# Kernel tuning notes

Hardware: AMD Instinct MI355X
Metric: run time of the kernel (lower is better)

Reference implementation:

```python
import jax, jax.numpy as jnp
import numpy as np

N, DIN, D, K0, NC = 32768, 768, 512, 128, 2
KS = [128, 64, 32, 16]  # prototype counts per stage (num_protos // 2**i)
NEG_SLOPE = 0.01


def _lin(x, W, b):
    # torch nn.Linear: W is [out, in]
    return x @ W.T + b


def _ln(x, g, b):
    m = x.mean(-1, keepdims=True)
    v = ((x - m) ** 2).mean(-1, keepdims=True)
    return (x - m) * jax.lax.rsqrt(v + 1e-5) * g + b


def setup_inputs() -> dict:
    key = jax.random.key(0)
    ks = jax.random.split(key, 40)
    s = 0.02

    def nrm(k, shp, sc=s):
        return jax.random.normal(k, shp, jnp.float32) * sc

    inp = {}
    inp["data"] = jax.random.normal(ks[0], (N, DIN), jnp.float32)
    inp["prototypes"] = jax.random.normal(ks[1], (K0, DIN), jnp.float32)
    inp["W_pp"] = nrm(ks[2], (D, DIN)); inp["b_pp"] = jnp.zeros((D,), jnp.float32)
    inp["W_cp"] = nrm(ks[3], (D, DIN)); inp["b_cp"] = jnp.zeros((D,), jnp.float32)
    inp["sim_scale"] = jnp.ones((1,), jnp.float32)
    # 3 enhancer MLPs + layernorms (stacked, same shapes)
    inp["enh_w1"] = nrm(ks[4], (3, D, D)); inp["enh_b1"] = jnp.zeros((3, D), jnp.float32)
    inp["enh_w2"] = nrm(ks[5], (3, D, D)); inp["enh_b2"] = jnp.zeros((3, D), jnp.float32)
    inp["ln_g"] = jnp.ones((3, D), jnp.float32); inp["ln_b"] = jnp.zeros((3, D), jnp.float32)
    # ProtoReducers: Mlp along K axis; fc1 [inK,inK], fc2 [outK,inK]
    ki = 6
    for i in range(3):
        inK, outK = KS[i], KS[i + 1]
        inp[f"red_w1_{i}"] = nrm(ks[ki], (inK, inK)); ki += 1
        inp[f"red_b1_{i}"] = jnp.zeros((inK,), jnp.float32)
        inp[f"red_w2_{i}"] = nrm(ks[ki], (outK, inK)); ki += 1
        inp[f"red_b2_{i}"] = jnp.zeros((outK,), jnp.float32)
    inp["W_proc"] = nrm(ks[20], (D, D)); inp["b_proc"] = jnp.zeros((D,), jnp.float32)
    inp["g_an"] = jnp.ones((D,), jnp.float32); inp["b_an"] = jnp.zeros((D,), jnp.float32)
    inp["W_t"] = nrm(ks[21], (D, D)); inp["b_t"] = jnp.zeros((D,), jnp.float32)
    inp["W_g"] = nrm(ks[22], (D, D)); inp["b_g"] = jnp.zeros((D,), jnp.float32)
    inp["W_s"] = nrm(ks[23], (1, D)); inp["b_s"] = jnp.zeros((1,), jnp.float32)
    inp["W_h"] = nrm(ks[24], (D, D)); inp["b_h"] = jnp.zeros((D,), jnp.float32)
    inp["W_c"] = nrm(ks[25], (NC, D)); inp["b_c"] = jnp.zeros((NC,), jnp.float32)
    return inp


def reference(data, prototypes, W_pp, b_pp, W_cp, b_cp, sim_scale,
              enh_w1, enh_b1, enh_w2, enh_b2, ln_g, ln_b,
              red_w1_0, red_b1_0, red_w2_0, red_b2_0,
              red_w1_1, red_b1_1, red_w2_1, red_b2_1,
              red_w1_2, red_b1_2, red_w2_2, red_b2_2,
              W_proc, b_proc, g_an, b_an,
              W_t, b_t, W_g, b_g, W_s, b_s, W_h, b_h, W_c, b_c):
    # patch / prototype projections (Linear + LeakyReLU)
    P = jax.nn.leaky_relu(_lin(data, W_pp, b_pp), NEG_SLOPE)        # [N, D]
    C = jax.nn.leaky_relu(_lin(prototypes, W_cp, b_cp), NEG_SLOPE)  # [K0, D]
    # denom = max(1e-6, tau * similarity_scale.item()); tau=1, no grad through scale
    denom = jnp.maximum(1e-6, jax.lax.stop_gradient(sim_scale)[0])
    reds = [(red_w1_0, red_b1_0, red_w2_0, red_b2_0),
            (red_w1_1, red_b1_1, red_w2_1, red_b2_1),
            (red_w1_2, red_b1_2, red_w2_2, red_b2_2)]
    for i in range(3):
        # L2 similarity: -cdist(P, C) computed as a GEMM
        d2 = (jnp.sum(P * P, -1, keepdims=True) + jnp.sum(C * C, -1)[None, :]
              - 2.0 * (P @ C.T))
        sim = -jnp.sqrt(jnp.maximum(d2, 1e-12))                     # [N, K]
        A = jax.nn.softmax(sim / denom, axis=1)                     # soft routing
        ctx = A @ C                                                 # [N, D]
        P = _ln(P + ctx, ln_g[i], ln_b[i])
        P = P + _lin(jax.nn.relu(_lin(P, enh_w1[i], enh_b1[i])), enh_w2[i], enh_b2[i])
        # ProtoReducer: Mlp over K axis (operate on C.T of shape [D, K])
        w1, b1, w2, b2 = reds[i]
        Ct = _lin(jax.nn.relu(_lin(C.T, w1, b1)), w2, b2)           # [D, Kout]
        C = Ct.T
    Z = jnp.concatenate([P, C], axis=0)                             # [N+16, D]
    Z = jax.nn.relu(_lin(Z, W_proc, b_proc))
    Z = _ln(Z, g_an, b_an)
    # gated attention MIL pooling
    t = jnp.tanh(_lin(Z, W_t, b_t))
    g = jax.nn.sigmoid(_lin(Z, W_g, b_g))
    scores = _lin(t * g, W_s, b_s)                                  # [N+16, 1]
    Aw = jax.nn.softmax(scores, axis=0)
    bag = Aw.T @ Z                                                  # [1, D]
    h = jax.nn.relu(_lin(bag, W_h, b_h))
    logits = _lin(h, W_c, b_c)                                      # [1, 2]
    return logits
```

## Files before the change

kernel.cpp:

```cpp
#include <hip/hip_runtime.h>
#include <math.h>

typedef _Float16 f16x8 __attribute__((ext_vector_type(8)));
typedef _Float16 f16x4 __attribute__((ext_vector_type(4)));
typedef float f32x4 __attribute__((ext_vector_type(4)));

#define TBM 256
#define TBN 128
#define TBK 32

#define AS1 __attribute__((address_space(1)))
#define AS3 __attribute__((address_space(3)))

__device__ __forceinline__ void gll16(const _Float16* g, _Float16* l)
{
    __builtin_amdgcn_global_load_lds((const AS1 unsigned int*)g,
                                     (AS3 unsigned int*)l, 16, 0, 0);
}

__device__ __forceinline__ int xcd_swz(int d, int nwg)
{
    int q = nwg >> 3, r = nwg & 7;
    int x = d & 7, idx = d >> 3;
    int base = x < r ? x * (q + 1) : r * (q + 1) + (x - r) * q;
    return base + idx;
}

__device__ __forceinline__ float fsigmoid(float x)
{
    return __builtin_amdgcn_rcpf(1.f + __expf(-x));
}
__device__ __forceinline__ float ftanh(float x)
{
    float ax = fabsf(x);
    float e = __expf(-2.f * ax);
    float t = (1.f - e) * __builtin_amdgcn_rcpf(1.f + e);
    return copysignf(t, x);
}

template<int ACT, bool F16OUT>
__global__ __launch_bounds__(256)
void dot_k(const float* __restrict__ X, const float* __restrict__ W,
           const float* __restrict__ bias, void* __restrict__ Yv,
           int M, int K)
{
    int gw = (blockIdx.x * 256 + threadIdx.x) >> 6;
    int lane = threadIdx.x & 63;
    if (gw >= M * 512) return;
    int r = gw >> 9, n = gw & 511;
    const float* xr = X + (size_t)r * K;
    const float* wr = W + (size_t)n * K;
    float d = 0.f;
    for (int t = 0; t < K; t += 256) {
        float4 a = *(const float4*)(xr + t + lane * 4);
        float4 b = *(const float4*)(wr + t + lane * 4);
        d += a.x * b.x + a.y * b.y + a.z * b.z + a.w * b.w;
    }
#pragma unroll
    for (int o = 32; o; o >>= 1) d += __shfl_xor(d, o);
    if (lane == 0) {
        float v = d + bias[n];
        if (ACT == 1) v = v > 0.f ? v : 0.01f * v;
        else if (ACT == 2) v = fmaxf(v, 0.f);
        if (F16OUT) ((_Float16*)Yv)[(size_t)r * 512 + n] = (_Float16)v;
        else        ((float*)Yv)[(size_t)r * 512 + n] = v;
    }
}

__global__ __launch_bounds__(256)
void cvtC2_k(const float* __restrict__ C, _Float16* __restrict__ Ch,
             _Float16* __restrict__ CTh, float* __restrict__ Csq, int Kin)
{
    int w = threadIdx.x >> 6, lane = threadIdx.x & 63;
    int row = blockIdx.x * 4 + w;
    if (row >= Kin) return;
    float4 a = *(const float4*)(C + (size_t)row * 512 + lane * 8);
    float4 b = *(const float4*)(C + (size_t)row * 512 + lane * 8 + 4);
    f16x8 h;
    h[0] = (_Float16)a.x; h[1] = (_Float16)a.y; h[2] = (_Float16)a.z; h[3] = (_Float16)a.w;
    h[4] = (_Float16)b.x; h[5] = (_Float16)b.y; h[6] = (_Float16)b.z; h[7] = (_Float16)b.w;
    *(f16x8*)(Ch + (size_t)row * 512 + lane * 8) = h;
    float s = 0.f;
#pragma unroll
    for (int q = 0; q < 8; q++) {
        float f = (float)h[q];
        s += f * f;
        CTh[(size_t)(lane * 8 + q) * Kin + row] = h[q];
    }
#pragma unroll
    for (int o = 32; o; o >>= 1) s += __shfl_xor(s, o);
    if (lane == 0) Csq[row] = s;
}

template<int MODE, int ACT, bool SQ>
__global__ __launch_bounds__(512)
void mgemm(const _Float16* __restrict__ A, const _Float16* __restrict__ B,
           const float* __restrict__ bias, _Float16* __restrict__ Yh,
           float* __restrict__ Psq, int M, int K, int Nout)
{
    __shared__ _Float16 As[2][TBM * TBK];
    __shared__ _Float16 Bs[2][TBN * TBK];
    const int tid = threadIdx.x;
    const int lane = tid & 63;
    const int wid = tid >> 6;
    const int wr = wid >> 1, wc = wid & 1;

    int bid = xcd_swz(blockIdx.y * gridDim.x + blockIdx.x, gridDim.x * gridDim.y);
    const int m0 = (bid / gridDim.x) * TBM;
    const int n0 = (bid % gridDim.x) * TBN;

    f32x4 acc[4][4] = {};
    const int nt = K / TBK;

    const int lrow = lane >> 2;
    const int lk = (lane & 3) * 8;

    auto stage = [&](int t, int buf) {
        const int k0 = t * TBK;
#pragma unroll
        for (int q = 0; q < 2; q++) {
            int c = wid * 2 + q;
            int r = c * 16 + lrow;
            int am = min(m0 + r, M - 1);
            gll16(A + (size_t)am * K + k0 + lk, &As[buf][c * 512]);
        }
        {
            int c = wid;
            int r = c * 16 + lrow;
            int bn = min(n0 + r, Nout - 1);
            gll16(B + (size_t)bn * K + k0 + lk, &Bs[buf][c * 512]);
        }
    };

    stage(0, 0);
    __syncthreads();
    for (int t = 0; t < nt; ++t) {
        const int cur = t & 1;
        if (t + 1 < nt) stage(t + 1, cur ^ 1);
        f16x8 af[4], bf[4];
#pragma unroll
        for (int mi = 0; mi < 4; mi++)
            af[mi] = *(const f16x8*)(&As[cur][(wr * 64 + mi * 16 + (lane & 15)) * TBK + (lane >> 4) * 8]);
#pragma unroll
        for (int nj = 0; nj < 4; nj++)
            bf[nj] = *(const f16x8*)(&Bs[cur][(wc * 64 + nj * 16 + (lane & 15)) * TBK + (lane >> 4) * 8]);
#pragma unroll
        for (int mi = 0; mi < 4; mi++)
#pragma unroll
            for (int nj = 0; nj < 4; nj++)
                acc[mi][nj] = __builtin_amdgcn_mfma_f32_16x16x32_f16(af[mi], bf[nj], acc[mi][nj], 0, 0, 0);
        __syncthreads();
    }

    _Float16* eb = &As[0][0];
    const int g = lane >> 4;
#pragma unroll
    for (int p = 0; p < 2; p++) {
        if (p) __syncthreads();
        if ((wr >> 1) == p) {
#pragma unroll
            for (int nj = 0; nj < 4; nj++) {
                int col = wc * 64 + nj * 16 + (lane & 15);
                float bv = bias ? bias[n0 + col] : 0.f;
#pragma unroll
                for (int mi = 0; mi < 4; mi++)
#pragma unroll
                    for (int r = 0; r < 4; r++) {
                        int lr = (wr & 1) * 64 + mi * 16 + g * 4 + r;
                        float v = acc[mi][nj][r] + bv;
                        if (MODE == 0) {
                            if (ACT == 1) v = v > 0.f ? v : 0.01f * v;
                            else if (ACT == 2) v = fmaxf(v, 0.f);
                        }
                        eb[lr * 128 + col] = (_Float16)v;
                    }
            }
        }
        __syncthreads();
        int t4 = tid * 4;
        int lr = t4 >> 4;
        int cbase = (t4 & 15) * 8;
        int m = m0 + p * 128 + lr;
        float sq = 0.f;
        if (m < M) {
#pragma unroll
            for (int q = 0; q < 4; q++) {
                int c0 = cbase + q * 8;
                f16x8 hv = *(f16x8*)(eb + lr * 128 + c0);
                size_t gidx = (size_t)m * Nout + n0 + c0;
                if (MODE == 1) {
                    f16x8 old = *(f16x8*)(Yh + gidx);
                    f16x8 nw;
#pragma unroll
                    for (int e = 0; e < 8; e++) {
                        float s = (float)old[e] + (float)hv[e];
                        nw[e] = (_Float16)s;
                    }
                    *(f16x8*)(Yh + gidx) = nw;
                    hv = nw;
                } else {
                    *(f16x8*)(Yh + gidx) = hv;
                }
                if (SQ) {
#pragma unroll
                    for (int e = 0; e < 8; e++) { float f = (float)hv[e]; sq += f * f; }
                }
            }
        }
        if (SQ) {
            sq += __shfl_xor(sq, 1);
            sq += __shfl_xor(sq, 2);
            if ((lane & 3) == 0 && m < M) atomicAdd(&Psq[m], sq);
        }
    }
}

__global__ __launch_bounds__(512)
void ctxln_k(const _Float16* __restrict__ A, const _Float16* __restrict__ CT,
             const float* __restrict__ g, const float* __restrict__ b,
             _Float16* __restrict__ Ph, int M, int Kin)
{
    __shared__ _Float16 As[2][128 * TBK];
    __shared__ _Float16 Bs[2][512 * TBK];
    const int tid = threadIdx.x;
    const int lane = tid & 63;
    const int wid = tid >> 6;
    const int wr = wid >> 2, wc = wid & 3;
    const int m0 = blockIdx.y * 128;

    f32x4 acc[4][8] = {};
    const int nt = Kin / TBK;

    const int lrow = lane >> 2;
    const int lk = (lane & 3) * 8;

    auto stage = [&](int t, int buf) {
        const int k0 = t * TBK;
        {
            int r = wid * 16 + lrow;
            gll16(A + (size_t)(m0 + r) * Kin + k0 + lk, &As[buf][wid * 512]);
        }
#pragma unroll
        for (int q = 0; q < 4; q++) {
            int c = wid * 4 + q;
            int n = c * 16 + lrow;
            gll16(CT + (size_t)n * Kin + k0 + lk, &Bs[buf][c * 512]);
        }
    };

    stage(0, 0);
    __syncthreads();
    for (int t = 0; t < nt; ++t) {
        const int cur = t & 1;
        if (t + 1 < nt) stage(t + 1, cur ^ 1);
        f16x8 af[4], bf[8];
#pragma unroll
        for (int mi = 0; mi < 4; mi++)
            af[mi] = *(const f16x8*)(&As[cur][(wr * 64 + mi * 16 + (lane & 15)) * TBK + (lane >> 4) * 8]);
#pragma unroll
        for (int nj = 0; nj < 8; nj++)
            bf[nj] = *(const f16x8*)(&Bs[cur][(wc * 128 + nj * 16 + (lane & 15)) * TBK + (lane >> 4) * 8]);
#pragma unroll
        for (int mi = 0; mi < 4; mi++)
#pragma unroll
            for (int nj = 0; nj < 8; nj++)
                acc[mi][nj] = __builtin_amdgcn_mfma_f32_16x16x32_f16(af[mi], bf[nj], acc[mi][nj], 0, 0, 0);
        __syncthreads();
    }

    _Float16* eb = &Bs[0][0];
    const int gq = lane >> 4;
#pragma unroll
    for (int p = 0; p < 2; p++) {
        if (p) __syncthreads();
        if (wr == p) {
#pragma unroll
            for (int nj = 0; nj < 8; nj++) {
                int col = wc * 128 + nj * 16 + (lane & 15);
#pragma unroll
                for (int mi = 0; mi < 4; mi++)
#pragma unroll
                    for (int r = 0; r < 4; r++) {
                        int lr = mi * 16 + gq * 4 + r;
                        eb[lr * 512 + col] = (_Float16)acc[mi][nj][r];
                    }
            }
        }
        __syncthreads();
#pragma unroll
        for (int rr = 0; rr < 8; rr++) {
            int lr = wid * 8 + rr;
            int m = m0 + p * 64 + lr;
            f16x8 cv = *(f16x8*)(eb + lr * 512 + lane * 8);
            f16x8 pv = *(const f16x8*)(Ph + (size_t)m * 512 + lane * 8);
            float v[8];
            float s = 0.f, ss = 0.f;
#pragma unroll
            for (int q = 0; q < 8; q++) {
                v[q] = (float)pv[q] + (float)cv[q];
                s += v[q]; ss += v[q] * v[q];
            }
#pragma unroll
            for (int o = 32; o; o >>= 1) { s += __shfl_xor(s, o); ss += __shfl_xor(ss, o); }
            float mean = s * (1.f / 512.f);
            float var = ss * (1.f / 512.f) - mean * mean;
            float inv = 1.f / sqrtf(var + 1e-5f);
            int d0 = lane * 8;
            f16x8 o8;
#pragma unroll
            for (int q = 0; q < 8; q++)
                o8[q] = (_Float16)((v[q] - mean) * inv * g[d0 + q] + b[d0 + q]);
            *(f16x8*)(Ph + (size_t)m * 512 + d0) = o8;
        }
    }
}

__global__ __launch_bounds__(512)
void procln_k(const _Float16* __restrict__ A, const _Float16* __restrict__ W,
              const float* __restrict__ bias, const float* __restrict__ g,
              const float* __restrict__ b, _Float16* __restrict__ Zh, int M)
{
    __shared__ _Float16 As[2][128 * TBK];
    __shared__ _Float16 Bs[2][512 * TBK];
    const int tid = threadIdx.x;
    const int lane = tid & 63;
    const int wid = tid >> 6;
    const int wr = wid >> 2, wc = wid & 3;
    const int m0 = blockIdx.y * 128;
    const int K = 512;

    f32x4 acc[4][8] = {};
    const int nt = K / TBK;

    const int lrow = lane >> 2;
    const int lk = (lane & 3) * 8;

    auto stage = [&](int t, int buf) {
        const int k0 = t * TBK;
        {
            int r = wid * 16 + lrow;
            gll16(A + (size_t)(m0 + r) * K + k0 + lk, &As[buf][wid * 512]);
        }
#pragma unroll
        for (int q = 0; q < 4; q++) {
            int c = wid * 4 + q;
            int n = c * 16 + lrow;
            gll16(W + (size_t)n * K + k0 + lk, &Bs[buf][c * 512]);
        }
    };

    stage(0, 0);
    __syncthreads();
    for (int t = 0; t < nt; ++t) {
        const int cur = t & 1;
        if (t + 1 < nt) stage(t + 1, cur ^ 1);
        f16x8 af[4], bf[8];
#pragma unroll
        for (int mi = 0; mi < 4; mi++)
            af[mi] = *(const f16x8*)(&As[cur][(wr * 64 + mi * 16 + (lane & 15)) * TBK + (lane >> 4) * 8]);
#pragma unroll
        for (int nj = 0; nj < 8; nj++)
            bf[nj] = *(const f16x8*)(&Bs[cur][(wc * 128 + nj * 16 + (lane & 15)) * TBK + (lane >> 4) * 8]);
#pragma unroll
        for (int mi = 0; mi < 4; mi++)
#pragma unroll
            for (int nj = 0; nj < 8; nj++)
                acc[mi][nj] = __builtin_amdgcn_mfma_f32_16x16x32_f16(af[mi], bf[nj], acc[mi][nj], 0, 0, 0);
        __syncthreads();
    }

    _Float16* eb = &Bs[0][0];
    const int gq = lane >> 4;
#pragma unroll
    for (int p = 0; p < 2; p++) {
        if (p) __syncthreads();
        if (wr == p) {
#pragma unroll
            for (int nj = 0; nj < 8; nj++) {
                int col = wc * 128 + nj * 16 + (lane & 15);
                float bv = bias[col];
#pragma unroll
                for (int mi = 0; mi < 4; mi++)
#pragma unroll
                    for (int r = 0; r < 4; r++) {
                        int lr = mi * 16 + gq * 4 + r;
                        eb[lr * 512 + col] = (_Float16)fmaxf(acc[mi][nj][r] + bv, 0.f);
                    }
            }
        }
        __syncthreads();
#pragma unroll
        for (int rr = 0; rr < 8; rr++) {
            int lr = wid * 8 + rr;
            int m = m0 + p * 64 + lr;
            f16x8 cv = *(f16x8*)(eb + lr * 512 + lane * 8);
            float v[8];
            float s = 0.f, ss = 0.f;
#pragma unroll
            for (int q = 0; q < 8; q++) {
                v[q] = (float)cv[q];
                s += v[q]; ss += v[q] * v[q];
            }
#pragma unroll
            for (int o = 32; o; o >>= 1) { s += __shfl_xor(s, o); ss += __shfl_xor(ss, o); }
            float mean = s * (1.f / 512.f);
            float var = ss * (1.f / 512.f) - mean * mean;
            float inv = 1.f / sqrtf(var + 1e-5f);
            int d0 = lane * 8;
            f16x8 o8;
#pragma unroll
            for (int q = 0; q < 8; q++)
                o8[q] = (_Float16)((v[q] - mean) * inv * g[d0 + q] + b[d0 + q]);
            *(f16x8*)(Zh + (size_t)m * 512 + d0) = o8;
        }
    }
}

__global__ __launch_bounds__(512)
void gatgemm(const _Float16* __restrict__ A, const _Float16* __restrict__ B1,
             const _Float16* __restrict__ B2, const float* __restrict__ c1,
             const float* __restrict__ c2, const float* __restrict__ Ws,
             float* __restrict__ scr, int M, int K, int Nout)
{
    __shared__ _Float16 As[2][TBM * TBK];
    __shared__ _Float16 B1s[2][TBN * TBK];
    __shared__ _Float16 B2s[2][TBN * TBK];
    const int tid = threadIdx.x;
    const int lane = tid & 63;
    const int wid = tid >> 6;
    const int wr = wid >> 1, wc = wid & 1;

    int bid = xcd_swz(blockIdx.y * gridDim.x + blockIdx.x, gridDim.x * gridDim.y);
    const int m0 = (bid / gridDim.x) * TBM;
    const int n0 = (bid % gridDim.x) * TBN;

    f32x4 acc1[4][4] = {};
    f32x4 acc2[4][4] = {};
    const int nt = K / TBK;

    const int lrow = lane >> 2;
    const int lk = (lane & 3) * 8;

    auto stage = [&](int t, int buf) {
        const int k0 = t * TBK;
#pragma unroll
        for (int q = 0; q < 2; q++) {
            int c = wid * 2 + q;
            int r = c * 16 + lrow;
            int am = min(m0 + r, M - 1);
            gll16(A + (size_t)am * K + k0 + lk, &As[buf][c * 512]);
        }
        {
            int c = wid;
            int r = c * 16 + lrow;
            int bn = min(n0 + r, Nout - 1);
            gll16(B1 + (size_t)bn * K + k0 + lk, &B1s[buf][c * 512]);
            gll16(B2 + (size_t)bn * K + k0 + lk, &B2s[buf][c * 512]);
        }
    };

    stage(0, 0);
    __syncthreads();
    for (int t = 0; t < nt; ++t) {
        const int cur = t & 1;
        if (t + 1 < nt) stage(t + 1, cur ^ 1);
        f16x8 af[4], bf1[4], bf2[4];
#pragma unroll
        for (int mi = 0; mi < 4; mi++)
            af[mi] = *(const f16x8*)(&As[cur][(wr * 64 + mi * 16 + (lane & 15)) * TBK + (lane >> 4) * 8]);
#pragma unroll
        for (int nj = 0; nj < 4; nj++) {
            int ro = (wc * 64 + nj * 16 + (lane & 15)) * TBK + (lane >> 4) * 8;
            bf1[nj] = *(const f16x8*)(&B1s[cur][ro]);
            bf2[nj] = *(const f16x8*)(&B2s[cur][ro]);
        }
#pragma unroll
        for (int mi = 0; mi < 4; mi++)
#pragma unroll
            for (int nj = 0; nj < 4; nj++) {
                acc1[mi][nj] = __builtin_amdgcn_mfma_f32_16x16x32_f16(af[mi], bf1[nj], acc1[mi][nj], 0, 0, 0);
                acc2[mi][nj] = __builtin_amdgcn_mfma_f32_16x16x32_f16(af[mi], bf2[nj], acc2[mi][nj], 0, 0, 0);
            }
        __syncthreads();
    }

    const int g = lane >> 4;
    float wsv[4];
#pragma unroll
    for (int nj = 0; nj < 4; nj++)
        wsv[nj] = Ws[n0 + wc * 64 + nj * 16 + (lane & 15)];
#pragma unroll
    for (int mi = 0; mi < 4; mi++) {
#pragma unroll
        for (int r = 0; r < 4; r++) {
            float p = 0.f;
#pragma unroll
            for (int nj = 0; nj < 4; nj++) {
                int col = n0 + wc * 64 + nj * 16 + (lane & 15);
                float t1 = ftanh(acc1[mi][nj][r] + c1[col]);
                float g1 = fsigmoid(acc2[mi][nj][r] + c2[col]);
                p += t1 * g1 * wsv[nj];
            }
#pragma unroll
            for (int o = 1; o < 16; o <<= 1) p += __shfl_xor(p, o);
            if ((lane & 15) == 0) {
                int m = m0 + wr * 64 + mi * 16 + g * 4 + r;
                if (m < M) atomicAdd(&scr[m], p);
            }
        }
    }
}

#define SBM 128
__global__ __launch_bounds__(256)
void simgemm(const _Float16* __restrict__ A, const _Float16* __restrict__ B,
             const float* __restrict__ Psq, const float* __restrict__ Csq,
             const float* __restrict__ sscale, _Float16* __restrict__ Ah,
             int M, int K, int Kin)
{
    __shared__ _Float16 As[2][SBM * TBK];
    __shared__ _Float16 Bs[2][SBM * TBK];
    __shared__ float redmx[2][SBM];
    __shared__ float redsm[2][SBM];
    const int tid = threadIdx.x;
    const int lane = tid & 63;
    const int wid = tid >> 6;
    const int wr = wid >> 1, wc = wid & 1;
    const int m0 = blockIdx.y * SBM;

    f32x4 acc[4][4] = {};
    const int nt = K / TBK;
    const int lrow = lane >> 2;
    const int lk = (lane & 3) * 8;

    auto stage = [&](int t, int buf) {
        const int k0 = t * TBK;
#pragma unroll
        for (int q = 0; q < 2; q++) {
            int c = wid * 2 + q;
            int r = c * 16 + lrow;
            int am = min(m0 + r, M - 1);
            gll16(A + (size_t)am * K + k0 + lk, &As[buf][c * 512]);
            if (c * 16 < Kin) {
                int bn = min(r, Kin - 1);
                gll16(B + (size_t)bn * K + k0 + lk, &Bs[buf][c * 512]);
            }
        }
    };

    stage(0, 0);
    __syncthreads();
    for (int t = 0; t < nt; ++t) {
        const int cur = t & 1;
        if (t + 1 < nt) stage(t + 1, cur ^ 1);
        f16x8 af[4], bf[4];
#pragma unroll
        for (int mi = 0; mi < 4; mi++)
            af[mi] = *(const f16x8*)(&As[cur][(wr * 64 + mi * 16 + (lane & 15)) * TBK + (lane >> 4) * 8]);
#pragma unroll
        for (int nj = 0; nj < 4; nj++)
            bf[nj] = *(const f16x8*)(&Bs[cur][(wc * 64 + nj * 16 + (lane & 15)) * TBK + (lane >> 4) * 8]);
#pragma unroll
        for (int mi = 0; mi < 4; mi++)
#pragma unroll
            for (int nj = 0; nj < 4; nj++)
                acc[mi][nj] = __builtin_amdgcn_mfma_f32_16x16x32_f16(af[mi], bf[nj], acc[mi][nj], 0, 0, 0);
        __syncthreads();
    }

    const float denom = fmaxf(1e-6f, sscale[0]);
    const int colbase = wc * 64 + (lane & 15);
    const int g = lane >> 4;
    float cc[4];
#pragma unroll
    for (int nj = 0; nj < 4; nj++) {
        int n = colbase + nj * 16;
        cc[nj] = (n < Kin) ? Csq[n] : 0.f;
    }

#pragma unroll
    for (int mi = 0; mi < 4; mi++) {
#pragma unroll
        for (int r = 0; r < 4; r++) {
            int row = wr * 64 + mi * 16 + g * 4 + r;
            float pp = Psq[m0 + row];
            float mx = -INFINITY;
#pragma unroll
            for (int nj = 0; nj < 4; nj++) {
                int n = colbase + nj * 16;
                float v = -INFINITY;
                if (n < Kin)
                    v = -sqrtf(fmaxf(pp + cc[nj] - 2.f * acc[mi][nj][r], 1e-12f)) / denom;
                acc[mi][nj][r] = v;
                mx = fmaxf(mx, v);
            }
#pragma unroll
            for (int o = 1; o < 16; o <<= 1) mx = fmaxf(mx, __shfl_xor(mx, o));
            if ((lane & 15) == 0) redmx[wc][row] = mx;
        }
    }
    __syncthreads();

#pragma unroll
    for (int mi = 0; mi < 4; mi++) {
#pragma unroll
        for (int r = 0; r < 4; r++) {
            int row = wr * 64 + mi * 16 + g * 4 + r;
            float mx = fmaxf(redmx[0][row], redmx[1][row]);
            float s = 0.f;
#pragma unroll
            for (int nj = 0; nj < 4; nj++) {
                int n = colbase + nj * 16;
                float e = (n < Kin) ? __expf(acc[mi][nj][r] - mx) : 0.f;
                acc[mi][nj][r] = e;
                s += e;
            }
#pragma unroll
            for (int o = 1; o < 16; o <<= 1) s += __shfl_xor(s, o);
            if ((lane & 15) == 0) redsm[wc][row] = s;
        }
    }
    __syncthreads();

#pragma unroll
    for (int mi = 0; mi < 4; mi++) {
#pragma unroll
        for (int r = 0; r < 4; r++) {
            int row = wr * 64 + mi * 16 + g * 4 + r;
            float inv = __builtin_amdgcn_rcpf(redsm[0][row] + redsm[1][row]);
            int m = m0 + row;
#pragma unroll
            for (int nj = 0; nj < 4; nj++) {
                int n = colbase + nj * 16;
                if (n < Kin)
                    Ah[(size_t)m * Kin + n] = (_Float16)(acc[mi][nj][r] * inv);
            }
        }
    }
}

__global__ __launch_bounds__(256)
void cvt_k(const float* __restrict__ x, _Float16* __restrict__ y, int n)
{
    int i = (blockIdx.x * 256 + threadIdx.x) * 4;
    if (i < n) {
        float4 v = *(const float4*)(x + i);
        f16x4 h = { (_Float16)v.x, (_Float16)v.y, (_Float16)v.z, (_Float16)v.w };
        *(f16x4*)(y + i) = h;
    }
}

__global__ __launch_bounds__(256)
void ln_k(const _Float16* __restrict__ X, const _Float16* __restrict__ R,
          const float* __restrict__ g, const float* __restrict__ b,
          _Float16* __restrict__ Yh, int M)
{
    int wid = threadIdx.x >> 6, lane = threadIdx.x & 63;
    int row = blockIdx.x * 4 + wid;
    if (row >= M) return;
    f16x8 a = *(const f16x8*)(X + (size_t)row * 512 + lane * 8);
    float v[8];
#pragma unroll
    for (int q = 0; q < 8; q++) v[q] = (float)a[q];
    if (R) {
        f16x8 c = *(const f16x8*)(R + (size_t)row * 512 + lane * 8);
#pragma unroll
        for (int q = 0; q < 8; q++) v[q] += (float)c[q];
    }
    float s = 0.f, ss = 0.f;
#pragma unroll
    for (int q = 0; q < 8; q++) { s += v[q]; ss += v[q] * v[q]; }
#pragma unroll
    for (int o = 32; o; o >>= 1) { s += __shfl_xor(s, o); ss += __shfl_xor(ss, o); }
    float mean = s * (1.f / 512.f);
    float var = ss * (1.f / 512.f) - mean * mean;
    float inv = 1.f / sqrtf(var + 1e-5f);
    int d0 = lane * 8;
    f16x8 o8;
#pragma unroll
    for (int q = 0; q < 8; q++)
        o8[q] = (_Float16)((v[q] - mean) * inv * g[d0 + q] + b[d0 + q]);
    *(f16x8*)(Yh + (size_t)row * 512 + d0) = o8;
}

__global__ __launch_bounds__(256)
void red1_k(const float* __restrict__ C, const float* __restrict__ w1,
            const float* __restrict__ b1, float* __restrict__ H1, int Kin)
{
    int d = blockIdx.x * 256 + threadIdx.x;
    int j = blockIdx.y;
    float acc = b1[j];
    for (int k = 0; k < Kin; k++) acc = fmaf(C[(size_t)k * 512 + d], w1[(size_t)j * Kin + k], acc);
    H1[(size_t)j * 512 + d] = fmaxf(acc, 0.f);
}

__global__ __launch_bounds__(256)
void red2_k(const float* __restrict__ H1, const float* __restrict__ w2,
            const float* __restrict__ b2, float* __restrict__ Cn,
            _Float16* __restrict__ Chn, _Float16* __restrict__ CThn,
            float* __restrict__ Csqn, int Kin, int Kout)
{
    int d = blockIdx.x * 256 + threadIdx.x;
    int j2 = blockIdx.y;
    float acc = b2[j2];
    for (int j = 0; j < Kin; j++) acc = fmaf(H1[(size_t)j * 512 + d], w2[(size_t)j2 * Kin + j], acc);
    Cn[(size_t)j2 * 512 + d] = acc;
    _Float16 h = (_Float16)acc;
    Chn[(size_t)j2 * 512 + d] = h;
    CThn[(size_t)d * Kout + j2] = h;
    float f = (float)h;
    float sq = f * f;
#pragma unroll
    for (int o = 32; o; o >>= 1) sq += __shfl_xor(sq, o);
    if ((threadIdx.x & 63) == 0) atomicAdd(&Csqn[j2], sq);
}

__global__ __launch_bounds__(1024)
void pool_k(float* __restrict__ s, float* __restrict__ scal, int M)
{
    __shared__ float sm[16];
    int tid = threadIdx.x, lane = tid & 63, wid = tid >> 6;
    float mx = -INFINITY;
    for (int i = tid * 4; i < M; i += 4096) {
        float4 a = *(const float4*)(s + i);
        mx = fmaxf(fmaxf(fmaxf(mx, a.x), fmaxf(a.y, a.z)), a.w);
    }
#pragma unroll
    for (int o = 32; o; o >>= 1) mx = fmaxf(mx, __shfl_xor(mx, o));
    if (lane == 0) sm[wid] = mx;
    __syncthreads();
    if (wid == 0) {
        float v = (lane < 16) ? sm[lane] : -INFINITY;
#pragma unroll
        for (int o = 8; o; o >>= 1) v = fmaxf(v, __shfl_xor(v, o));
        if (lane == 0) sm[0] = v;
    }
    __syncthreads();
    float gmax = sm[0];
    __syncthreads();
    float sum = 0.f;
    for (int i = tid * 4; i < M; i += 4096) {
        float4 a = *(const float4*)(s + i);
        float4 e;
        e.x = __expf(a.x - gmax); e.y = __expf(a.y - gmax);
        e.z = __expf(a.z - gmax); e.w = __expf(a.w - gmax);
        *(float4*)(s + i) = e;
        sum += e.x + e.y + e.z + e.w;
    }
#pragma unroll
    for (int o = 32; o; o >>= 1) sum += __shfl_xor(sum, o);
    if (lane == 0) sm[wid] = sum;
    __syncthreads();
    if (tid == 0) {
        float t = 0.f;
        for (int w = 0; w < 16; w++) t += sm[w];
        scal[0] = t;
    }
}

__global__ __launch_bounds__(256)
void bagp_k(const _Float16* __restrict__ Z, const float* __restrict__ w,
            float* __restrict__ PB, int M, int cs)
{
    int d = blockIdx.x * 256 + threadIdx.x;
    int chunk = blockIdx.y;
    int i0 = chunk * cs;
    int i1 = min(M, i0 + cs);
    float acc = 0.f;
    for (int i = i0; i < i1; i++) acc = fmaf(w[i], (float)Z[(size_t)i * 512 + d], acc);
    PB[(size_t)chunk * 512 + d] = acc;
}

__global__ __launch_bounds__(256)
void bagf_k(const float* __restrict__ PB, const float* __restrict__ scal,
            float* __restrict__ bag, int nchunk)
{
    int d = blockIdx.x * 256 + threadIdx.x;
    float acc = 0.f;
    for (int c = 0; c < nchunk; c++) acc += PB[(size_t)c * 512 + d];
    bag[d] = acc / scal[0];
}

__global__ __launch_bounds__(256)
void h_k(const float* __restrict__ bag, const float* __restrict__ Wh,
         const float* __restrict__ bh, float* __restrict__ h)
{
    int wid = threadIdx.x >> 6, lane = threadIdx.x & 63;
    int j = blockIdx.x * 4 + wid;
    const float* wr = Wh + (size_t)j * 512;
    float d = 0.f;
#pragma unroll
    for (int t = 0; t < 2; t++) {
        float4 a = *(const float4*)(wr + t * 256 + lane * 4);
        float4 bv = *(const float4*)(bag + t * 256 + lane * 4);
        d += a.x * bv.x + a.y * bv.y + a.z * bv.z + a.w * bv.w;
    }
#pragma unroll
    for (int o = 32; o; o >>= 1) d += __shfl_xor(d, o);
    if (lane == 0) h[j] = fmaxf(d + bh[j], 0.f);
}

__global__ __launch_bounds__(128)
void logit_k(const float* __restrict__ h, const float* __restrict__ Wc,
             const float* __restrict__ bc, float* __restrict__ out)
{
    int wid = threadIdx.x >> 6, lane = threadIdx.x & 63;
    const float* wr = Wc + (size_t)wid * 512;
    float d = 0.f;
#pragma unroll
    for (int t = 0; t < 2; t++) {
        float4 a = *(const float4*)(wr + t * 256 + lane * 4);
        float4 hv = *(const float4*)(h + t * 256 + lane * 4);
        d += a.x * hv.x + a.y * hv.y + a.z * hv.z + a.w * hv.w;
    }
#pragma unroll
    for (int o = 32; o; o >>= 1) d += __shfl_xor(d, o);
    if (lane == 0) out[wid] = d + bc[wid];
}

extern "C" void kernel_launch(void* const* d_in, const int* in_sizes, int n_in,
                              void* d_out, int out_size, void* d_ws, size_t ws_size,
                              hipStream_t stream)
{
    const float* data    = (const float*)d_in[0];
    const float* protos  = (const float*)d_in[1];
    const float* W_pp    = (const float*)d_in[2];
    const float* b_pp    = (const float*)d_in[3];
    const float* W_cp    = (const float*)d_in[4];
    const float* b_cp    = (const float*)d_in[5];
    const float* sscale  = (const float*)d_in[6];
    const float* enh_w1  = (const float*)d_in[7];
    const float* enh_b1  = (const float*)d_in[8];
    const float* enh_w2  = (const float*)d_in[9];
    const float* enh_b2  = (const float*)d_in[10];
    const float* ln_g    = (const float*)d_in[11];
    const float* ln_b    = (const float*)d_in[12];
    const float* red_w1[3] = {(const float*)d_in[13], (const float*)d_in[17], (const float*)d_in[21]};
    const float* red_b1[3] = {(const float*)d_in[14], (const float*)d_in[18], (const float*)d_in[22]};
    const float* red_w2[3] = {(const float*)d_in[15], (const float*)d_in[19], (const float*)d_in[23]};
    const float* red_b2[3] = {(const float*)d_in[16], (const float*)d_in[20], (const float*)d_in[24]};
    const float* W_proc  = (const float*)d_in[25];
    const float* b_proc  = (const float*)d_in[26];
    const float* g_an    = (const float*)d_in[27];
    const float* b_an    = (const float*)d_in[28];
    const float* W_t     = (const float*)d_in[29];
    const float* b_t     = (const float*)d_in[30];
    const float* W_g     = (const float*)d_in[31];
    const float* b_g     = (const float*)d_in[32];
    const float* W_s     = (const float*)d_in[33];
    const float* b_s     = (const float*)d_in[34];
    const float* W_h     = (const float*)d_in[35];
    const float* b_h     = (const float*)d_in[36];
    const float* W_c     = (const float*)d_in[37];
    const float* b_c     = (const float*)d_in[38];
    float* out = (float*)d_out;
    (void)b_s;

    constexpr int N = 32768, DIN = 768, D = 512;
    constexpr int NCHUNK = 256;
    char* w = (char*)d_ws;
    auto alloc = [&](size_t bytes) -> char* {
        char* p = w; w += (bytes + 255) & ~(size_t)255; return p;
    };
    _Float16* Ph     = (_Float16*)alloc((size_t)N * D * 2);
    _Float16* TMPh   = (_Float16*)alloc((size_t)N * D * 2);
    _Float16* Zh     = (_Float16*)alloc((size_t)(N + 16) * D * 2);
    _Float16* Ztail  = (_Float16*)alloc((size_t)16 * D * 2);
    _Float16* datah  = (_Float16*)alloc((size_t)N * DIN * 2);
    _Float16* Ah     = (_Float16*)alloc((size_t)N * 128 * 2);
    _Float16* Ch     = (_Float16*)alloc(128 * D * 2);
    _Float16* CTh    = (_Float16*)alloc(128 * D * 2);
    _Float16* Wpph   = (_Float16*)alloc((size_t)D * DIN * 2);
    _Float16* w1h    = (_Float16*)alloc((size_t)3 * D * D * 2);
    _Float16* w2h    = (_Float16*)alloc((size_t)3 * D * D * 2);
    _Float16* Wproch = (_Float16*)alloc((size_t)D * D * 2);
    _Float16* Wth    = (_Float16*)alloc((size_t)D * D * 2);
    _Float16* Wgh    = (_Float16*)alloc((size_t)D * D * 2);
    float*    Psq    = (float*)alloc((size_t)N * 4);
    float*    Csq    = (float*)alloc(128 * 4);
    float*    Ca     = (float*)alloc(128 * D * 4);
    float*    Cb     = (float*)alloc(128 * D * 4);
    float*    H1     = (float*)alloc(128 * D * 4);
    float*    scr    = (float*)alloc((size_t)(N + 16) * 4);
    float*    PB     = (float*)alloc((size_t)NCHUNK * D * 4);
    float*    bag    = (float*)alloc(D * 4);
    float*    hb     = (float*)alloc(D * 4);
    float*    scal   = (float*)alloc(8 * 4);

    dim3 blk(256);
    dim3 blk512(512);
    auto cgrid = [](size_t n) { return dim3((unsigned)((n / 4 + 255) / 256)); };
    auto mgrid = [](int M_, int Nout_) { return dim3((Nout_ + TBN - 1) / TBN, (M_ + TBM - 1) / TBM); };

    cvt_k<<<cgrid((size_t)N * DIN), blk, 0, stream>>>(data, datah, N * DIN);
    cvt_k<<<cgrid((size_t)D * DIN), blk, 0, stream>>>(W_pp, Wpph, D * DIN);
    cvt_k<<<cgrid((size_t)3 * D * D), blk, 0, stream>>>(enh_w1, w1h, 3 * D * D);
    cvt_k<<<cgrid((size_t)3 * D * D), blk, 0, stream>>>(enh_w2, w2h, 3 * D * D);
    cvt_k<<<cgrid((size_t)D * D), blk, 0, stream>>>(W_proc, Wproch, D * D);
    cvt_k<<<cgrid((size_t)D * D), blk, 0, stream>>>(W_t, Wth, D * D);
    cvt_k<<<cgrid((size_t)D * D), blk, 0, stream>>>(W_g, Wgh, D * D);

    hipMemsetAsync(Psq, 0, (size_t)N * 4, stream);
    mgemm<0, 1, true><<<mgrid(N, D), blk512, 0, stream>>>(datah, Wpph, b_pp, Ph, Psq, N, DIN, D);
    dot_k<1, false><<<dim3(128 * 512 / 4), blk, 0, stream>>>(protos, W_cp, b_cp, Ca, 128, DIN);
    cvtC2_k<<<dim3(32), blk, 0, stream>>>(Ca, Ch, CTh, Csq, 128);

    float* C = Ca;
    float* Cn = Cb;
    int Kin = 128;
    for (int i = 0; i < 3; i++) {
        int Kout = Kin >> 1;
        simgemm<<<dim3(1, N / SBM), blk, 0, stream>>>(Ph, Ch, Psq, Csq, sscale, Ah, N, D, Kin);
        if (i < 2) hipMemsetAsync(Psq, 0, (size_t)N * 4, stream);
        ctxln_k<<<dim3(1, N / 128), blk512, 0, stream>>>(Ah, CTh, ln_g + (size_t)i * D, ln_b + (size_t)i * D, Ph, N, Kin);
        mgemm<0, 2, false><<<mgrid(N, D), blk512, 0, stream>>>(Ph, w1h + (size_t)i * D * D, enh_b1 + (size_t)i * D, TMPh, nullptr, N, D, D);
        if (i < 2)
            mgemm<1, 0, true><<<mgrid(N, D), blk512, 0, stream>>>(TMPh, w2h + (size_t)i * D * D, enh_b2 + (size_t)i * D, Ph, Psq, N, D, D);
        else
            mgemm<1, 0, false><<<mgrid(N, D), blk512, 0, stream>>>(TMPh, w2h + (size_t)i * D * D, enh_b2 + (size_t)i * D, Ph, nullptr, N, D, D);
        hipMemsetAsync(Csq, 0, 128 * 4, stream);
        red1_k<<<dim3(2, Kin), blk, 0, stream>>>(C, red_w1[i], red_b1[i], H1, Kin);
        red2_k<<<dim3(2, Kout), blk, 0, stream>>>(H1, red_w2[i], red_b2[i], Cn, Ch, CTh, Csq, Kin, Kout);
        float* t = C; C = Cn; Cn = t;
        Kin = Kout;
    }

    procln_k<<<dim3(1, N / 128), blk512, 0, stream>>>(Ph, Wproch, b_proc, g_an, b_an, Zh, N);
    dot_k<2, true><<<dim3(16 * 512 / 4), blk, 0, stream>>>(C, W_proc, b_proc, Ztail, 16, D);
    ln_k<<<dim3(4), blk, 0, stream>>>(Ztail, nullptr, g_an, b_an, Zh + (size_t)N * D, 16);

    hipMemsetAsync(scr, 0, (size_t)(N + 16) * 4, stream);
    gatgemm<<<mgrid(N + 16, D), blk512, 0, stream>>>(Zh, Wth, Wgh, b_t, b_g, W_s, scr, N + 16, D, D);

    pool_k<<<dim3(1), dim3(1024), 0, stream>>>(scr, scal, N + 16);
    int cs = (N + 16 + NCHUNK - 1) / NCHUNK;
    bagp_k<<<dim3(2, NCHUNK), blk, 0, stream>>>(Zh, scr, PB, N + 16, cs);
    bagf_k<<<dim3(2), blk, 0, stream>>>(PB, scal, bag, NCHUNK);

    h_k<<<dim3(128), blk, 0, stream>>>(bag, W_h, b_h, hb);
    logit_k<<<dim3(1), dim3(128), 0, stream>>>(hb, W_c, b_c, out);
}
```

Measured before the change: 794.8 us.

## Replace atomics with partial-sum slots, merge conversions, specialize small similarity GEMMs

Seven fp32-to-fp16 conversion launches become one grid-stride kernel driven by a segment table. Row-norm and gated-score atomics are replaced by per-column-tile partial slots (4 per row) that readers sum, which also removes several memset launches. Stage 2 and 3 similarity GEMMs get a templated kernel sized to the actual prototype count, with 256-row tiles and no masked columns. The partial-slot buffers add extra memory traffic, and pool_k now reads float4 partials serially per element.

After: 772.5 us. -2.8%, faster.

```diff
diff --git a/kernel.cpp b/kernel.cpp
--- a/kernel.cpp
+++ b/kernel.cpp
@@ -36,6 +36,26 @@
     float e = __expf(-2.f * ax);
     float t = (1.f - e) * __builtin_amdgcn_rcpf(1.f + e);
     return copysignf(t, x);
+}
+
+struct CvtSegs {
+    const float* src[7];
+    _Float16* dst[7];
+    int cum4[8];
+};
+
+__global__ __launch_bounds__(256)
+void cvtall_k(CvtSegs a)
+{
+    int total = a.cum4[7];
+    for (int i = blockIdx.x * 256 + threadIdx.x; i < total; i += gridDim.x * 256) {
+        int s = 0;
+        while (i >= a.cum4[s + 1]) s++;
+        int loc = (i - a.cum4[s]) * 4;
+        float4 v = *(const float4*)(a.src[s] + loc);
+        f16x4 h = { (_Float16)v.x, (_Float16)v.y, (_Float16)v.z, (_Float16)v.w };
+        *(f16x4*)(a.dst[s] + loc) = h;
+    }
 }
 
 template<int ACT, bool F16OUT>
@@ -69,7 +89,7 @@
 
 __global__ __launch_bounds__(256)
 void cvtC2_k(const float* __restrict__ C, _Float16* __restrict__ Ch,
-             _Float16* __restrict__ CTh, float* __restrict__ Csq, int Kin)
+             _Float16* __restrict__ CTh, float* __restrict__ Csq2, int Kin)
 {
     int w = threadIdx.x >> 6, lane = threadIdx.x & 63;
     int row = blockIdx.x * 4 + w;
@@ -89,14 +109,14 @@
     }
 #pragma unroll
     for (int o = 32; o; o >>= 1) s += __shfl_xor(s, o);
-    if (lane == 0) Csq[row] = s;
+    if (lane == 0) { Csq2[row * 2] = s; Csq2[row * 2 + 1] = 0.f; }
 }
 
 template<int MODE, int ACT, bool SQ>
 __global__ __launch_bounds__(512)
 void mgemm(const _Float16* __restrict__ A, const _Float16* __restrict__ B,
            const float* __restrict__ bias, _Float16* __restrict__ Yh,
-           float* __restrict__ Psq, int M, int K, int Nout)
+           float* __restrict__ Psq4, int M, int K, int Nout)
 {
     __shared__ _Float16 As[2][TBM * TBK];
     __shared__ _Float16 Bs[2][TBN * TBK];
@@ -210,7 +230,7 @@
         if (SQ) {
             sq += __shfl_xor(sq, 1);
             sq += __shfl_xor(sq, 2);
-            if ((lane & 3) == 0 && m < M) atomicAdd(&Psq[m], sq);
+            if ((lane & 3) == 0 && m < M) Psq4[(size_t)m * 4 + (n0 >> 7)] = sq;
         }
     }
 }
@@ -420,7 +440,7 @@
 void gatgemm(const _Float16* __restrict__ A, const _Float16* __restrict__ B1,
              const _Float16* __restrict__ B2, const float* __restrict__ c1,
              const float* __restrict__ c2, const float* __restrict__ Ws,
-             float* __restrict__ scr, int M, int K, int Nout)
+             float* __restrict__ scr4, int M, int K, int Nout)
 {
     __shared__ _Float16 As[2][TBM * TBK];
     __shared__ _Float16 B1s[2][TBN * TBK];
@@ -505,7 +525,7 @@
             for (int o = 1; o < 16; o <<= 1) p += __shfl_xor(p, o);
             if ((lane & 15) == 0) {
                 int m = m0 + wr * 64 + mi * 16 + g * 4 + r;
-                if (m < M) atomicAdd(&scr[m], p);
+                if (m < M) scr4[(size_t)m * 4 + (n0 >> 7)] = p;
             }
         }
     }
@@ -514,10 +534,11 @@
 #define SBM 128
 __global__ __launch_bounds__(256)
 void simgemm(const _Float16* __restrict__ A, const _Float16* __restrict__ B,
-             const float* __restrict__ Psq, const float* __restrict__ Csq,
+             const float* __restrict__ Psq4, const float* __restrict__ Csq2,
              const float* __restrict__ sscale, _Float16* __restrict__ Ah,
-             int M, int K, int Kin)
-{
+             int M, int K)
+{
+    const int Kin = 128;
     __shared__ _Float16 As[2][SBM * TBK];
     __shared__ _Float16 Bs[2][SBM * TBK];
     __shared__ float redmx[2][SBM];
@@ -539,12 +560,8 @@
         for (int q = 0; q < 2; q++) {
             int c = wid * 2 + q;
             int r = c * 16 + lrow;
-            int am = min(m0 + r, M - 1);
-            gll16(A + (size_t)am * K + k0 + lk, &As[buf][c * 512]);
-            if (c * 16 < Kin) {
-                int bn = min(r, Kin - 1);
-                gll16(B + (size_t)bn * K + k0 + lk, &Bs[buf][c * 512]);
-            }
+            gll16(A + (size_t)(m0 + r) * K + k0 + lk, &As[buf][c * 512]);
+            gll16(B + (size_t)r * K + k0 + lk, &Bs[buf][c * 512]);
         }
     };
 
@@ -575,7 +592,7 @@
 #pragma unroll
     for (int nj = 0; nj < 4; nj++) {
         int n = colbase + nj * 16;
-        cc[nj] = (n < Kin) ? Csq[n] : 0.f;
+        cc[nj] = Csq2[n * 2] + Csq2[n * 2 + 1];
     }
 
 #pragma unroll
@@ -583,14 +600,12 @@
 #pragma unroll
         for (int r = 0; r < 4; r++) {
             int row = wr * 64 + mi * 16 + g * 4 + r;
-            float pp = Psq[m0 + row];
+            float4 pq = *(const float4*)(Psq4 + (size_t)(m0 + row) * 4);
+            float pp = (pq.x + pq.y) + (pq.z + pq.w);
             float mx = -INFINITY;
 #pragma unroll
             for (int nj = 0; nj < 4; nj++) {
-                int n = colbase + nj * 16;
-                float v = -INFINITY;
-                if (n < Kin)
-                    v = -sqrtf(fmaxf(pp + cc[nj] - 2.f * acc[mi][nj][r], 1e-12f)) / denom;
+                float v = -sqrtf(fmaxf(pp + cc[nj] - 2.f * acc[mi][nj][r], 1e-12f)) / denom;
                 acc[mi][nj][r] = v;
                 mx = fmaxf(mx, v);
             }
@@ -610,8 +625,7 @@
             float s = 0.f;
 #pragma unroll
             for (int nj = 0; nj < 4; nj++) {
-                int n = colbase + nj * 16;
-                float e = (n < Kin) ? __expf(acc[mi][nj][r] - mx) : 0.f;
+                float e = __expf(acc[mi][nj][r] - mx);
                 acc[mi][nj][r] = e;
                 s += e;
             }
@@ -630,23 +644,102 @@
             float inv = __builtin_amdgcn_rcpf(redsm[0][row] + redsm[1][row]);
             int m = m0 + row;
 #pragma unroll
-            for (int nj = 0; nj < 4; nj++) {
-                int n = colbase + nj * 16;
-                if (n < Kin)
-                    Ah[(size_t)m * Kin + n] = (_Float16)(acc[mi][nj][r] * inv);
-            }
-        }
-    }
-}
-
+            for (int nj = 0; nj < 4; nj++)
+                Ah[(size_t)m * Kin + colbase + nj * 16] = (_Float16)(acc[mi][nj][r] * inv);
+        }
+    }
+}
+
+template<int KIN>
 __global__ __launch_bounds__(256)
-void cvt_k(const float* __restrict__ x, _Float16* __restrict__ y, int n)
-{
-    int i = (blockIdx.x * 256 + threadIdx.x) * 4;
-    if (i < n) {
-        float4 v = *(const float4*)(x + i);
-        f16x4 h = { (_Float16)v.x, (_Float16)v.y, (_Float16)v.z, (_Float16)v.w };
-        *(f16x4*)(y + i) = h;
+void simgemm_s(const _Float16* __restrict__ A, const _Float16* __restrict__ B,
+               const float* __restrict__ Psq4, const float* __restrict__ Csq2,
+               const float* __restrict__ sscale, _Float16* __restrict__ Ah,
+               int M, int K)
+{
+    constexpr int NB = KIN / 16;
+    __shared__ _Float16 As[2][256 * TBK];
+    __shared__ _Float16 Bs[2][KIN * TBK];
+    const int tid = threadIdx.x;
+    const int lane = tid & 63;
+    const int wid = tid >> 6;
+    const int m0 = blockIdx.y * 256;
+
+    f32x4 acc[4][NB] = {};
+    const int nt = K / TBK;
+    const int lrow = lane >> 2;
+    const int lk = (lane & 3) * 8;
+
+    auto stage = [&](int t, int buf) {
+        const int k0 = t * TBK;
+#pragma unroll
+        for (int q = 0; q < 4; q++) {
+            int c = wid * 4 + q;
+            int r = c * 16 + lrow;
+            gll16(A + (size_t)(m0 + r) * K + k0 + lk, &As[buf][c * 512]);
+        }
+        if (wid < NB) {
+            int r = wid * 16 + lrow;
+            gll16(B + (size_t)r * K + k0 + lk, &Bs[buf][wid * 512]);
+        }
+    };
+
+    stage(0, 0);
+    __syncthreads();
+    for (int t = 0; t < nt; ++t) {
+        const int cur = t & 1;
+        if (t + 1 < nt) stage(t + 1, cur ^ 1);
+        f16x8 af[4], bf[NB];
+#pragma unroll
+        for (int mi = 0; mi < 4; mi++)
+            af[mi] = *(const f16x8*)(&As[cur][(wid * 64 + mi * 16 + (lane & 15)) * TBK + (lane >> 4) * 8]);
+#pragma unroll
+        for (int nj = 0; nj < NB; nj++)
+            bf[nj] = *(const f16x8*)(&Bs[cur][(nj * 16 + (lane & 15)) * TBK + (lane >> 4) * 8]);
+#pragma unroll
+        for (int mi = 0; mi < 4; mi++)
+#pragma unroll
+            for (int nj = 0; nj < NB; nj++)
+                acc[mi][nj] = __builtin_amdgcn_mfma_f32_16x16x32_f16(af[mi], bf[nj], acc[mi][nj], 0, 0, 0);
+        __syncthreads();
+    }
+
+    const float denom = fmaxf(1e-6f, sscale[0]);
+    const int g = lane >> 4;
+    float cc[NB];
+#pragma unroll
+    for (int nj = 0; nj < NB; nj++) {
+        int n = nj * 16 + (lane & 15);
+        cc[nj] = Csq2[n * 2] + Csq2[n * 2 + 1];
+    }
+
+#pragma unroll
+    for (int mi = 0; mi < 4; mi++) {
+#pragma unroll
+        for (int r = 0; r < 4; r++) {
+            int m = m0 + wid * 64 + mi * 16 + g * 4 + r;
+            float4 pq = *(const float4*)(Psq4 + (size_t)m * 4);
+            float pp = (pq.x + pq.y) + (pq.z + pq.w);
+            float vv[NB];
+            float mx = -INFINITY;
+#pragma unroll
+            for (int nj = 0; nj < NB; nj++) {
+                float v = -sqrtf(fmaxf(pp + cc[nj] - 2.f * acc[mi][nj][r], 1e-12f)) / denom;
+                vv[nj] = v;
+                mx = fmaxf(mx, v);
+            }
+#pragma unroll
+            for (int o = 1; o < 16; o <<= 1) mx = fmaxf(mx, __shfl_xor(mx, o));
+            float s = 0.f;
+#pragma unroll
+            for (int nj = 0; nj < NB; nj++) { float e = __expf(vv[nj] - mx); vv[nj] = e; s += e; }
+#pragma unroll
+            for (int o = 1; o < 16; o <<= 1) s += __shfl_xor(s, o);
+            float inv = __builtin_amdgcn_rcpf(s);
+#pragma unroll
+            for (int nj = 0; nj < NB; nj++)
+                Ah[(size_t)m * KIN + nj * 16 + (lane & 15)] = (_Float16)(vv[nj] * inv);
+        }
     }
 }
 
@@ -698,8 +791,9 @@
 void red2_k(const float* __restrict__ H1, const float* __restrict__ w2,
             const float* __restrict__ b2, float* __restrict__ Cn,
             _Float16* __restrict__ Chn, _Float16* __restrict__ CThn,
-            float* __restrict__ Csqn, int Kin, int Kout)
-{
+            float* __restrict__ Csq2, int Kin, int Kout)
+{
+    __shared__ float sm[4];
     int d = blockIdx.x * 256 + threadIdx.x;
     int j2 = blockIdx.y;
     float acc = b2[j2];
@@ -712,18 +806,24 @@
     float sq = f * f;
 #pragma unroll
     for (int o = 32; o; o >>= 1) sq += __shfl_xor(sq, o);
-    if ((threadIdx.x & 63) == 0) atomicAdd(&Csqn[j2], sq);
+    if ((threadIdx.x & 63) == 0) sm[threadIdx.x >> 6] = sq;
+    __syncthreads();
+    if (threadIdx.x == 0)
+        Csq2[j2 * 2 + blockIdx.x] = (sm[0] + sm[1]) + (sm[2] + sm[3]);
 }
 
 __global__ __launch_bounds__(1024)
-void pool_k(float* __restrict__ s, float* __restrict__ scal, int M)
+void pool_k(const float4* __restrict__ s4, float* __restrict__ s,
+            float* __restrict__ scal, int M)
 {
     __shared__ float sm[16];
     int tid = threadIdx.x, lane = tid & 63, wid = tid >> 6;
     float mx = -INFINITY;
-    for (int i = tid * 4; i < M; i += 4096) {
-        float4 a = *(const float4*)(s + i);
-        mx = fmaxf(fmaxf(fmaxf(mx, a.x), fmaxf(a.y, a.z)), a.w);
+    for (int i = tid; i < M; i += 1024) {
+        float4 a = s4[i];
+        float v = (a.x + a.y) + (a.z + a.w);
+        s[i] = v;
+        mx = fmaxf(mx, v);
     }
 #pragma unroll
     for (int o = 32; o; o >>= 1) mx = fmaxf(mx, __shfl_xor(mx, o));
@@ -739,13 +839,10 @@
     float gmax = sm[0];
     __syncthreads();
     float sum = 0.f;
-    for (int i = tid * 4; i < M; i += 4096) {
-        float4 a = *(const float4*)(s + i);
-        float4 e;
-        e.x = __expf(a.x - gmax); e.y = __expf(a.y - gmax);
-        e.z = __expf(a.z - gmax); e.w = __expf(a.w - gmax);
-        *(float4*)(s + i) = e;
-        sum += e.x + e.y + e.z + e.w;
+    for (int i = tid; i < M; i += 1024) {
+        float e = __expf(s[i] - gmax);
+        s[i] = e;
+        sum += e;
     }
 #pragma unroll
     for (int o = 32; o; o >>= 1) sum += __shfl_xor(sum, o);
@@ -876,11 +973,12 @@
     _Float16* Wproch = (_Float16*)alloc((size_t)D * D * 2);
     _Float16* Wth    = (_Float16*)alloc((size_t)D * D * 2);
     _Float16* Wgh    = (_Float16*)alloc((size_t)D * D * 2);
-    float*    Psq    = (float*)alloc((size_t)N * 4);
-    float*    Csq    = (float*)alloc(128 * 4);
+    float*    Psq4   = (float*)alloc((size_t)N * 4 * 4);
+    float*    Csq2   = (float*)alloc(128 * 2 * 4);
     float*    Ca     = (float*)alloc(128 * D * 4);
     float*    Cb     = (float*)alloc(128 * D * 4);
     float*    H1     = (float*)alloc(128 * D * 4);
+    float*    scr4   = (float*)alloc((size_t)(N + 16) * 4 * 4);
     float*    scr    = (float*)alloc((size_t)(N + 16) * 4);
     float*    PB     = (float*)alloc((size_t)NCHUNK * D * 4);
     float*    bag    = (float*)alloc(D * 4);
@@ -889,38 +987,46 @@
 
     dim3 blk(256);
     dim3 blk512(512);
-    auto cgrid = [](size_t n) { return dim3((unsigned)((n / 4 + 255) / 256)); };
     auto mgrid = [](int M_, int Nout_) { return dim3((Nout_ + TBN - 1) / TBN, (M_ + TBM - 1) / TBM); };
 
-    cvt_k<<<cgrid((size_t)N * DIN), blk, 0, stream>>>(data, datah, N * DIN);
-    cvt_k<<<cgrid((size_t)D * DIN), blk, 0, stream>>>(W_pp, Wpph, D * DIN);
-    cvt_k<<<cgrid((size_t)3 * D * D), blk, 0, stream>>>(enh_w1, w1h, 3 * D * D);
-    cvt_k<<<cgrid((size_t)3 * D * D), blk, 0, stream>>>(enh_w2, w2h, 3 * D * D);
-    cvt_k<<<cgrid((size_t)D * D), blk, 0, stream>>>(W_proc, Wproch, D * D);
-    cvt_k<<<cgrid((size_t)D * D), blk, 0, stream>>>(W_t, Wth, D * D);
-    cvt_k<<<cgrid((size_t)D * D), blk, 0, stream>>>(W_g, Wgh, D * D);
-
-    hipMemsetAsync(Psq, 0, (size_t)N * 4, stream);
-    mgemm<0, 1, true><<<mgrid(N, D), blk512, 0, stream>>>(datah, Wpph, b_pp, Ph, Psq, N, DIN, D);
+    {
+        CvtSegs cs;
+        const float* srcs[7] = { data, W_pp, enh_w1, enh_w2, W_proc, W_t, W_g };
+        _Float16* dsts[7]    = { datah, Wpph, w1h, w2h, Wproch, Wth, Wgh };
+        int sizes[7] = { N * DIN, D * DIN, 3 * D * D, 3 * D * D, D * D, D * D, D * D };
+        int c = 0;
+        cs.cum4[0] = 0;
+        for (int s = 0; s < 7; s++) {
+            cs.src[s] = srcs[s]; cs.dst[s] = dsts[s];
+            c += sizes[s] / 4;
+            cs.cum4[s + 1] = c;
+        }
+        cvtall_k<<<dim3(4096), blk, 0, stream>>>(cs);
+    }
+
+    mgemm<0, 1, true><<<mgrid(N, D), blk512, 0, stream>>>(datah, Wpph, b_pp, Ph, Psq4, N, DIN, D);
     dot_k<1, false><<<dim3(128 * 512 / 4), blk, 0, stream>>>(protos, W_cp, b_cp, Ca, 128, DIN);
-    cvtC2_k<<<dim3(32), blk, 0, stream>>>(Ca, Ch, CTh, Csq, 128);
+    cvtC2_k<<<dim3(32), blk, 0, stream>>>(Ca, Ch, CTh, Csq2, 128);
 
     float* C = Ca;
     float* Cn = Cb;
     int Kin = 128;
     for (int i = 0; i < 3; i++) {
         int Kout = Kin >> 1;
-        simgemm<<<dim3(1, N / SBM), blk, 0, stream>>>(Ph, Ch, Psq, Csq, sscale, Ah, N, D, Kin);
-        if (i < 2) hipMemsetAsync(Psq, 0, (size_t)N * 4, stream);
+        if (i == 0)
+            simgemm<<<dim3(1, N / SBM), blk, 0, stream>>>(Ph, Ch, Psq4, Csq2, sscale, Ah, N, D);
+        else if (i == 1)
+            simgemm_s<64><<<dim3(1, N / 256), blk, 0, stream>>>(Ph, Ch, Psq4, Csq2, sscale, Ah, N, D);
+        else
+            simgemm_s<32><<<dim3(1, N / 256), blk, 0, stream>>>(Ph, Ch, Psq4, Csq2, sscale, Ah, N, D);
         ctxln_k<<<dim3(1, N / 128), blk512, 0, stream>>>(Ah, CTh, ln_g + (size_t)i * D, ln_b + (size_t)i * D, Ph, N, Kin);
         mgemm<0, 2, false><<<mgrid(N, D), blk512, 0, stream>>>(Ph, w1h + (size_t)i * D * D, enh_b1 + (size_t)i * D, TMPh, nullptr, N, D, D);
         if (i < 2)
-            mgemm<1, 0, true><<<mgrid(N, D), blk512, 0, stream>>>(TMPh, w2h + (size_t)i * D * D, enh_b2 + (size_t)i * D, Ph, Psq, N, D, D);
+            mgemm<1, 0, true><<<mgrid(N, D), blk512, 0, stream>>>(TMPh, w2h + (size_t)i * D * D, enh_b2 + (size_t)i * D, Ph, Psq4, N, D, D);
         else
             mgemm<1, 0, false><<<mgrid(N, D), blk512, 0, stream>>>(TMPh, w2h + (size_t)i * D * D, enh_b2 + (size_t)i * D, Ph, nullptr, N, D, D);
-        hipMemsetAsync(Csq, 0, 128 * 4, stream);
         red1_k<<<dim3(2, Kin), blk, 0, stream>>>(C, red_w1[i], red_b1[i], H1, Kin);
-        red2_k<<<dim3(2, Kout), blk, 0, stream>>>(H1, red_w2[i], red_b2[i], Cn, Ch, CTh, Csq, Kin, Kout);
+        red2_k<<<dim3(2, Kout), blk, 0, stream>>>(H1, red_w2[i], red_b2[i], Cn, Ch, CTh, Csq2, Kin, Kout);
         float* t = C; C = Cn; Cn = t;
         Kin = Kout;
     }
@@ -929,12 +1035,11 @@
     dot_k<2, true><<<dim3(16 * 512 / 4), blk, 0, stream>>>(C, W_proc, b_proc, Ztail, 16, D);
     ln_k<<<dim3(4), blk, 0, stream>>>(Ztail, nullptr, g_an, b_an, Zh + (size_t)N * D, 16);
 
-    hipMemsetAsync(scr, 0, (size_t)(N + 16) * 4, stream);
-    gatgemm<<<mgrid(N + 16, D), blk512, 0, stream>>>(Zh, Wth, Wgh, b_t, b_g, W_s, scr, N + 16, D, D);
-
-    pool_k<<<dim3(1), dim3(1024), 0, stream>>>(scr, scal, N + 16);
-    int cs = (N + 16 + NCHUNK - 1) / NCHUNK;
-    bagp_k<<<dim3(2, NCHUNK), blk, 0, stream>>>(Zh, scr, PB, N + 16, cs);
+    gatgemm<<<mgrid(N + 16, D), blk512, 0, stream>>>(Zh, Wth, Wgh, b_t, b_g, W_s, scr4, N + 16, D, D);
+
+    pool_k<<<dim3(1), dim3(1024), 0, stream>>>((const float4*)scr4, scr, scal, N + 16);
+    int cs2 = (N + 16 + NCHUNK - 1) / NCHUNK;
+    bagp_k<<<dim3(2, NCHUNK), blk, 0, stream>>>(Zh, scr, PB, N + 16, cs2);
     bagf_k<<<dim3(2), blk, 0, stream>>>(PB, scal, bag, NCHUNK);
 
     h_k<<<dim3(128), blk, 0, stream>>>(bag, W_h, b_h, hb);
```
